# Kernel tuning notes

Hardware: AMD Instinct MI355X
Metric: run time of the kernel (lower is better)

Reference implementation:

```python
import math
import jax, jax.numpy as jnp
import numpy as np

N_HEAD = 16
ROPE_BASE = 10000.0

def setup_inputs() -> dict:
    key = jax.random.key(0)
    k1, k2, k3 = jax.random.split(key, 3)
    B, T, C = 2, 2048, 2048
    x = jax.random.normal(k1, (B, T, C), dtype=jnp.float32)
    Wqkv = jax.random.normal(k2, (C, 3 * C), dtype=jnp.float32) * 0.02  # [C, 3C], y = x @ Wqkv
    Wout = jax.random.normal(k3, (C, C), dtype=jnp.float32) * 0.02
    return {"x": x, "Wqkv": Wqkv, "Wout": Wout}

def _rope_sin_cos(T, half, dtype):
    # build_sin_cos(seq_len, dim=head_size//2): div over arange(0, 2*dim, 2) / (2*dim)
    pos = jnp.arange(T, dtype=jnp.float32)[:, None]                      # [T,1]
    div = jnp.exp(jnp.arange(0, 2 * half, 2, dtype=jnp.float32)
                  * (-math.log(ROPE_BASE) / (2 * half)))                 # [half]
    ang = pos * div                                                      # [T,half]
    return jnp.sin(ang).astype(dtype), jnp.cos(ang).astype(dtype)

def reference(x, Wqkv, Wout):
    B, T, C = x.shape
    H = N_HEAD
    D = C // H
    half = D // 2
    qkv = (x @ Wqkv).reshape(B, T, 3, H, D)
    q, k, v = qkv[:, :, 0], qkv[:, :, 1], qkv[:, :, 2]                   # [B,T,H,D]
    sin, cos = _rope_sin_cos(T, half, x.dtype)
    sin = sin[None, :, None, :]  # [1,T,1,half]
    cos = cos[None, :, None, :]
    def rope(t):
        t1, t2 = t[..., :half], t[..., half:]
        return jnp.concatenate([t1 * cos - t2 * sin, t2 * cos + t1 * sin], axis=-1)
    q, k = rope(q), rope(k)
    scale = 1.0 / math.sqrt(D)  # flash-attn default softmax_scale
    scores = jnp.einsum('bthd,bshd->bhts', q, k) * scale                 # [B,H,T,T]
    causal = jnp.tril(jnp.ones((T, T), dtype=bool))
    scores = jnp.where(causal[None, None], scores, jnp.finfo(scores.dtype).min)
    probs = jax.nn.softmax(scores, axis=-1)
    out = jnp.einsum('bhts,bshd->bhtd', probs, v)                        # [B,H,T,D]
    # Faithful to torch: out.permute(0,2,1,3).reshape(B,T,C) on [B,T,H,D]
    # == flatten of [B,H,T,D] into [B,T,C]
    out = out.reshape(B, T, C)
    return out @ Wout
```

## Files before the change

### kernel.cpp

```cpp
#include <hip/hip_runtime.h>

typedef unsigned short u16;
typedef __attribute__((ext_vector_type(8))) short bf16x8;
typedef __attribute__((ext_vector_type(4))) float f32x4;
typedef __attribute__((ext_vector_type(8))) unsigned short u16x8;

#define B_ 2
#define T_ 2048
#define C_ 2048
#define H_ 16
#define D_ 128
#define QKVW 6144

__device__ __forceinline__ u16 f2b(float f) {
  unsigned int x = __builtin_bit_cast(unsigned int, f);
  x += 0x7fffu + ((x >> 16) & 1u);
  return (u16)(x >> 16);
}
__device__ __forceinline__ float b2f(u16 u) {
  unsigned int x = ((unsigned int)u) << 16;
  return __builtin_bit_cast(float, x);
}
__device__ __forceinline__ void gl_lds16(const void* g, void* l) {
  __builtin_amdgcn_global_load_lds((const __attribute__((address_space(1))) void*)g,
                                   (__attribute__((address_space(3))) void*)l, 16, 0, 0);
}

__global__ void castbf(const float* __restrict__ in, u16* __restrict__ out) {
  int i = blockIdx.x * 256 + threadIdx.x;
  f32x4 a = ((const f32x4*)in)[2 * i];
  f32x4 b = ((const f32x4*)in)[2 * i + 1];
  u16x8 o;
  o[0] = f2b(a[0]); o[1] = f2b(a[1]); o[2] = f2b(a[2]); o[3] = f2b(a[3]);
  o[4] = f2b(b[0]); o[5] = f2b(b[1]); o[6] = f2b(b[2]); o[7] = f2b(b[3]);
  ((u16x8*)out)[i] = o;
}

__global__ __launch_bounds__(256) void castT(const float* __restrict__ in,
                                             u16* __restrict__ out, int K, int N) {
  __shared__ __align__(16) u16 ld[64][72];
  const int nt = blockIdx.x * 64, kt = blockIdx.y * 64;
  const int tid = threadIdx.x;
#pragma unroll
  for (int s = 0; s < 4; ++s) {
    int idx = tid + s * 256;
    int r = idx >> 4;
    int c = (idx & 15) * 4;
    f32x4 v = *(const f32x4*)(in + (size_t)(kt + r) * N + nt + c);
    ld[r][c] = f2b(v[0]); ld[r][c + 1] = f2b(v[1]);
    ld[r][c + 2] = f2b(v[2]); ld[r][c + 3] = f2b(v[3]);
  }
  __syncthreads();
#pragma unroll
  for (int s = 0; s < 2; ++s) {
    int idx = tid + s * 256;
    int n = idx >> 3;
    int c8 = (idx & 7) * 8;
    u16x8 o;
#pragma unroll
    for (int j = 0; j < 8; ++j) o[j] = ld[c8 + j][n];
    *(u16x8*)(out + (size_t)(nt + n) * K + kt + c8) = o;
  }
}

__device__ __forceinline__ void stage_chunk(const u16* __restrict__ g, int K,
                                            u16* l, int ch) {
  int row = ch >> 3;
  int c = (ch & 7) ^ (row & 7);
  gl_lds16(g + (size_t)row * K + c * 8, l + ch * 8);
}

#define MFMA_Q(AF, BF, MH, NH)                                               \
  _Pragma("unroll")                                                          \
  for (int mi = 0; mi < 4; ++mi) {                                           \
    _Pragma("unroll")                                                        \
    for (int ni = 0; ni < 2; ++ni) {                                         \
      _Pragma("unroll")                                                      \
      for (int ks = 0; ks < 2; ++ks)                                         \
        acc[(MH)*4 + mi][(NH)*2 + ni] =                                      \
            __builtin_amdgcn_mfma_f32_16x16x32_bf16(                         \
                AF[mi][ks], BF[ni][ks], acc[(MH)*4 + mi][(NH)*2 + ni],       \
                0, 0, 0);                                                    \
    }                                                                        \
  }

template <int OUT_BF16>
__global__ __launch_bounds__(512, 2) void gemm256(const u16* __restrict__ A,
                                                  const u16* __restrict__ Bt,
                                                  void* __restrict__ Cout,
                                                  int M, int N, int K) {
  __shared__ __align__(16) u16 sm[65536];
  const int tid = threadIdx.x;
  const int lane = tid & 63, w = tid >> 6;
  const int quad = lane >> 4, l15 = lane & 15;
  const int wm = w >> 2, wn = w & 3;
  const int NXT = N >> 8;
  int id = blockIdx.x;
  const int cpx = gridDim.x >> 3;
  id = (id & 7) * cpx + (id >> 3);
  const int tn0 = (id % NXT) * 256, tm0 = (id / NXT) * 256;
  const int NT = K >> 6;
  const u16* Ag = A + (size_t)tm0 * K;
  const u16* Bg = Bt + (size_t)tn0 * K;

  f32x4 acc[8][4] = {};
  bf16x8 a0[4][2], a1[4][2], b0[2][2], b1[2][2];

  auto stA = [&](int tt, int half) {
    u16* l = &sm[(tt & 1) * 32768];
    const u16* g = Ag + tt * 64;
    stage_chunk(g, K, l, half * 512 + tid);
    stage_chunk(g, K, l, 1024 + half * 512 + tid);
  };
  auto stB = [&](int tt, int nh) {
    u16* l = &sm[(tt & 1) * 32768 + 16384];
    const u16* g = Bg + tt * 64;
    int ch = nh * 256 + (tid & 255) + ((tid >> 8) << 9);
    stage_chunk(g, K, l, ch);
    stage_chunk(g, K, l, ch + 1024);
  };

  stA(0, 0); stB(0, 0); stA(0, 1); stB(0, 1);
  if (NT > 1) {
    stA(1, 0); stB(1, 0); stA(1, 1);
    asm volatile("s_waitcnt vmcnt(6)" ::: "memory");
  } else {
    asm volatile("s_waitcnt vmcnt(0)" ::: "memory");
  }
  __builtin_amdgcn_s_barrier();

  for (int t = 0; t < NT; ++t) {
    const u16* LA = &sm[(t & 1) * 32768];
    const u16* LB = LA + 16384;
#pragma unroll
    for (int mi = 0; mi < 4; ++mi)
#pragma unroll
      for (int ks = 0; ks < 2; ++ks) {
        int r = wm * 128 + mi * 16 + l15;
        a0[mi][ks] = *(const bf16x8*)&LA[r * 64 +
                     ((ks * 32 + quad * 8) ^ ((r & 7) << 3))];
      }
#pragma unroll
    for (int ni = 0; ni < 2; ++ni)
#pragma unroll
      for (int ks = 0; ks < 2; ++ks) {
        int r = wn * 64 + ni * 16 + l15;
        b0[ni][ks] = *(const bf16x8*)&LB[r * 64 +
                     ((ks * 32 + quad * 8) ^ ((r & 7) << 3))];
      }
    if (t + 1 < NT) stB(t + 1, 1);
    __builtin_amdgcn_s_barrier();
    asm volatile("s_waitcnt lgkmcnt(0)");
    __builtin_amdgcn_sched_barrier(0);
    __builtin_amdgcn_s_setprio(1);
    MFMA_Q(a0, b0, 0, 0);
    __builtin_amdgcn_s_setprio(0);
    __builtin_amdgcn_s_barrier();
#pragma unroll
    for (int ni = 0; ni < 2; ++ni)
#pragma unroll
      for (int ks = 0; ks < 2; ++ks) {
        int r = wn * 64 + (ni + 2) * 16 + l15;
        b1[ni][ks] = *(const bf16x8*)&LB[r * 64 +
                     ((ks * 32 + quad * 8) ^ ((r & 7) << 3))];
      }
    if (t + 2 < NT) stA(t + 2, 0);
    __builtin_amdgcn_s_barrier();
    asm volatile("s_waitcnt lgkmcnt(0)");
    __builtin_amdgcn_sched_barrier(0);
    __builtin_amdgcn_s_setprio(1);
    MFMA_Q(a0, b1, 0, 1);
    __builtin_amdgcn_s_setprio(0);
    __builtin_amdgcn_s_barrier();
#pragma unroll
    for (int mi = 0; mi < 4; ++mi)
#pragma unroll
      for (int ks = 0; ks < 2; ++ks) {
        int r = wm * 128 + (mi + 4) * 16 + l15;
        a1[mi][ks] = *(const bf16x8*)&LA[r * 64 +
                     ((ks * 32 + quad * 8) ^ ((r & 7) << 3))];
      }
    if (t + 2 < NT) stB(t + 2, 0);
    __builtin_amdgcn_s_barrier();
    asm volatile("s_waitcnt lgkmcnt(0)");
    __builtin_amdgcn_sched_barrier(0);
    __builtin_amdgcn_s_setprio(1);
    MFMA_Q(a1, b1, 1, 1);
    __builtin_amdgcn_s_setprio(0);
    __builtin_amdgcn_s_barrier();
    if (t + 2 < NT) {
      stA(t + 2, 1);
      asm volatile("s_waitcnt vmcnt(6)" ::: "memory");
    } else {
      asm volatile("s_waitcnt vmcnt(0)" ::: "memory");
    }
    __builtin_amdgcn_s_barrier();
    __builtin_amdgcn_s_setprio(1);
    MFMA_Q(a1, b0, 1, 0);
    __builtin_amdgcn_s_setprio(0);
    __builtin_amdgcn_s_barrier();
  }

#pragma unroll
  for (int mi = 0; mi < 8; ++mi)
#pragma unroll
    for (int ni = 0; ni < 4; ++ni)
#pragma unroll
      for (int r = 0; r < 4; ++r) {
        int row = tm0 + wm * 128 + mi * 16 + quad * 4 + r;
        int col = tn0 + wn * 64 + ni * 16 + l15;
        float v = acc[mi][ni][r];
        if (OUT_BF16) ((u16*)Cout)[(size_t)row * N + col] = f2b(v);
        else          ((float*)Cout)[(size_t)row * N + col] = v;
      }
}

__global__ void rope_k(u16* __restrict__ qkv) {
  int g = blockIdx.x * 256 + threadIdx.x;
  int i0 = (g & 7) * 8;
  int h = (g >> 3) & 15;
  int which = (g >> 7) & 1;
  int t = (g >> 8) & 2047;
  int b = g >> 19;
  size_t base = (size_t)(b * T_ + t) * QKVW + which * 2048 + h * 128 + i0;
  u16x8 v1 = *(const u16x8*)(qkv + base);
  u16x8 v2 = *(const u16x8*)(qkv + base + 64);
  u16x8 o1, o2;
#pragma unroll
  for (int j = 0; j < 8; ++j) {
    int i = i0 + j;
    float t1 = b2f(v1[j]), t2 = b2f(v2[j]);
    float ang = (float)t * exp2f(-(float)i * 0.20762050593046439f);
    float sn, cs;
    sincosf(ang, &sn, &cs);
    o1[j] = f2b(t1 * cs - t2 * sn);
    o2[j] = f2b(t2 * cs + t1 * sn);
  }
  *(u16x8*)(qkv + base) = o1;
  *(u16x8*)(qkv + base + 64) = o2;
}

__global__ __launch_bounds__(256) void vtrans(const u16* __restrict__ qkv, u16* __restrict__ vt) {
  __shared__ __align__(16) u16 ld[128][136];
  const int tt = blockIdx.x, bh = blockIdx.y;
  const int b = bh >> 4, h = bh & 15;
  const u16* vb = qkv + (size_t)b * T_ * QKVW + 4096 + h * 128;
  const int tid = threadIdx.x;
#pragma unroll
  for (int s = 0; s < 8; ++s) {
    int t = (tid >> 4) + s * 16;
    int d0 = (tid & 15) * 8;
    *(bf16x8*)&ld[t][d0] = *(const bf16x8*)(vb + (size_t)(tt * 128 + t) * QKVW + d0);
  }
  __syncthreads();
  u16* vout = vt + (size_t)bh * D_ * T_ + tt * 128;
#pragma unroll
  for (int s = 0; s < 8; ++s) {
    int d = (tid >> 4) + s * 16;
    int t0 = (tid & 15) * 8;
    u16x8 o;
#pragma unroll
    for (int j = 0; j < 8; ++j) o[j] = ld[t0 + j][d];
    *(u16x8*)(vout + (size_t)d * T_ + t0) = o;
  }
}

#define APW 72
__global__ __launch_bounds__(256, 2) void attn(const u16* __restrict__ qkv,
                                               const u16* __restrict__ vt,
                                               u16* __restrict__ obuf) {
  __shared__ __align__(16) u16 lK[2][64 * 128];
  __shared__ __align__(16) u16 lV[2][128 * 64];
  __shared__ __align__(16) u16 lP[64 * APW];
  const int tid = threadIdx.x, lane = tid & 63, w = tid >> 6;
  const int quad = lane >> 4, l15 = lane & 15;
  const int bh = blockIdx.x, jp = blockIdx.y;
  const int jA = jp, jB = 31 - jp;
  const int b = bh >> 4, h = bh & 15;
  const u16* qb = qkv + (size_t)b * T_ * QKVW + h * 128;
  const u16* kb = qb + 2048;
  const u16* vtb = vt + (size_t)bh * D_ * T_;

  bf16x8 qfA[4], qfB[4];
#pragma unroll
  for (int kk = 0; kk < 4; ++kk) {
    qfA[kk] = *(const bf16x8*)(qb + (size_t)(jA * 64 + w * 16 + l15) * QKVW + kk * 32 + quad * 8);
    qfB[kk] = *(const bf16x8*)(qb + (size_t)(jB * 64 + w * 16 + l15) * QKVW + kk * 32 + quad * 8);
  }

  f32x4 oA[8] = {}, oB[8] = {};
  float mA[4], lAr[4], mB[4], lBr[4];
#pragma unroll
  for (int r = 0; r < 4; ++r) {
    mA[r] = -__builtin_inff(); lAr[r] = 0.f;
    mB[r] = -__builtin_inff(); lBr[r] = 0.f;
  }
  const float sc = 0.08838834764831845f * 1.4426950408889634f;

  auto stage = [&](int kt, int buf) {
#pragma unroll
    for (int s = 0; s < 4; ++s) {
      int ch = tid + s * 256;
      int kr = ch >> 4, kc = (ch & 15) ^ (kr & 7);
      gl_lds16(kb + (size_t)(kt * 64 + kr) * QKVW + kc * 8, &lK[buf][ch * 8]);
      int vr = ch >> 3, vc = (ch & 7) ^ (vr & 7);
      gl_lds16(vtb + (size_t)vr * T_ + kt * 64 + vc * 8, &lV[buf][ch * 8]);
    }
  };

  auto smpv = [&](f32x4* sacc, f32x4* oacc, float* mrow, float* lrow,
                  int jw, int kt, int cb) {
    const bool diag = (kt == jw);
#pragma unroll
    for (int nj = 0; nj < 4; ++nj) {
      int key = nj * 16 + l15;
#pragma unroll
      for (int r = 0; r < 4; ++r) {
        float s = sacc[nj][r] * sc;
        if (diag) {
          int qrow = w * 16 + quad * 4 + r;
          if (key > qrow) s = -__builtin_inff();
        }
        sacc[nj][r] = s;
      }
    }
    float pm[4];
#pragma unroll
    for (int r = 0; r < 4; ++r)
      pm[r] = fmaxf(fmaxf(sacc[0][r], sacc[1][r]), fmaxf(sacc[2][r], sacc[3][r]));
    float dmax = fmaxf(fmaxf(pm[0] - mrow[0], pm[1] - mrow[1]),
                       fmaxf(pm[2] - mrow[2], pm[3] - mrow[3]));
    if (__any(dmax > 11.5f)) {
#pragma unroll
      for (int r = 0; r < 4; ++r) {
        float rm = pm[r];
        rm = fmaxf(rm, __shfl_xor(rm, 1));
        rm = fmaxf(rm, __shfl_xor(rm, 2));
        rm = fmaxf(rm, __shfl_xor(rm, 4));
        rm = fmaxf(rm, __shfl_xor(rm, 8));
        float mold = mrow[r];
        float mnew = fmaxf(mold, rm);
        float alpha = exp2f(mold - mnew);
#pragma unroll
        for (int nd = 0; nd < 8; ++nd) oacc[nd][r] *= alpha;
        lrow[r] *= alpha;
        mrow[r] = mnew;
      }
    }
#pragma unroll
    for (int r = 0; r < 4; ++r) {
      int prow = w * 16 + quad * 4 + r;
      float rs = 0.f;
#pragma unroll
      for (int nj = 0; nj < 4; ++nj) {
        float p = exp2f(sacc[nj][r] - mrow[r]);
        rs += p;
        lP[prow * APW + nj * 16 + l15] = f2b(p);
      }
      lrow[r] += rs;
    }
#pragma unroll
    for (int kk = 0; kk < 2; ++kk) {
      bf16x8 pf, vf[8];
      pf = *(const bf16x8*)&lP[(w * 16 + l15) * APW + kk * 32 + quad * 8];
#pragma unroll
      for (int nd = 0; nd < 8; ++nd) {
        int r = nd * 16 + l15;
        vf[nd] = *(const bf16x8*)&lV[cb][r * 64 + ((kk * 32 + quad * 8) ^ ((r & 7) << 3))];
      }
      __builtin_amdgcn_s_setprio(1);
#pragma unroll
      for (int nd = 0; nd < 8; ++nd)
        oacc[nd] = __builtin_amdgcn_mfma_f32_16x16x32_bf16(pf, vf[nd], oacc[nd], 0, 0, 0);
      __builtin_amdgcn_s_setprio(0);
    }
  };

  stage(0, 0);
  __syncthreads();

  for (int kt = 0; kt <= jB; ++kt) {
    int cb = kt & 1;
    if (kt < jB) stage(kt + 1, cb ^ 1);
    const bool doA = (kt <= jA);
    f32x4 sB[4] = {}, sA[4] = {};
#pragma unroll
    for (int kk = 0; kk < 4; ++kk) {
      bf16x8 kf[4];
#pragma unroll
      for (int nj = 0; nj < 4; ++nj) {
        int r = nj * 16 + l15;
        kf[nj] = *(const bf16x8*)&lK[cb][r * 128 + ((kk * 32 + quad * 8) ^ ((r & 7) << 3))];
      }
      __builtin_amdgcn_s_setprio(1);
#pragma unroll
      for (int nj = 0; nj < 4; ++nj)
        sB[nj] = __builtin_amdgcn_mfma_f32_16x16x32_bf16(qfB[kk], kf[nj], sB[nj], 0, 0, 0);
      if (doA)
#pragma unroll
        for (int nj = 0; nj < 4; ++nj)
          sA[nj] = __builtin_amdgcn_mfma_f32_16x16x32_bf16(qfA[kk], kf[nj], sA[nj], 0, 0, 0);
      __builtin_amdgcn_s_setprio(0);
    }
    smpv(sB, oB, mB, lBr, jB, kt, cb);
    if (doA) smpv(sA, oA, mA, lAr, jA, kt, cb);
    __syncthreads();
  }

#pragma unroll
  for (int r = 0; r < 4; ++r) {
    float sA = lAr[r], sB = lBr[r];
    sA += __shfl_xor(sA, 1); sB += __shfl_xor(sB, 1);
    sA += __shfl_xor(sA, 2); sB += __shfl_xor(sB, 2);
    sA += __shfl_xor(sA, 4); sB += __shfl_xor(sB, 4);
    sA += __shfl_xor(sA, 8); sB += __shfl_xor(sB, 8);
    lAr[r] = sA; lBr[r] = sB;
  }

#pragma unroll
  for (int nd = 0; nd < 8; ++nd)
#pragma unroll
    for (int r = 0; r < 4; ++r) {
      int dcol = nd * 16 + l15;
      int qrB = jB * 64 + w * 16 + quad * 4 + r;
      obuf[((size_t)bh * T_ + qrB) * D_ + dcol] = f2b(oB[nd][r] / lBr[r]);
      int qrA = jA * 64 + w * 16 + quad * 4 + r;
      obuf[((size_t)bh * T_ + qrA) * D_ + dcol] = f2b(oA[nd][r] / lAr[r]);
    }
}

extern "C" void kernel_launch(void* const* d_in, const int* in_sizes, int n_in,
                              void* d_out, int out_size, void* d_ws, size_t ws_size,
                              hipStream_t stream) {
  const float* x = (const float*)d_in[0];
  const float* Wqkv = (const float*)d_in[1];
  const float* Wout = (const float*)d_in[2];
  float* out = (float*)d_out;
  char* ws = (char*)d_ws;

  u16* xb   = (u16*)ws;
  u16* wqt  = (u16*)(ws + 16777216);
  u16* qkvb = (u16*)(ws + 41943040);
  u16* vtb  = (u16*)(ws + 92274688);
  u16* wot  = wqt;
  u16* ob   = xb;

  castbf<<<4096, 256, 0, stream>>>(x, xb);
  castT<<<dim3(96, 32), 256, 0, stream>>>(Wqkv, wqt, 2048, 6144);
  gemm256<1><<<dim3(384), 512, 0, stream>>>(xb, wqt, qkvb, 4096, 6144, 2048);
  castT<<<dim3(32, 32), 256, 0, stream>>>(Wout, wot, 2048, 2048);
  rope_k<<<4096, 256, 0, stream>>>(qkvb);
  vtrans<<<dim3(16, 32), 256, 0, stream>>>(qkvb, vtb);
  attn<<<dim3(32, 16), 256, 0, stream>>>(qkvb, vtb, ob);
  gemm256<0><<<dim3(128), 512, 0, stream>>>(ob, wot, out, 4096, 2048, 2048);
}
```

Baseline: 400.7 us.

## Add 128x256-tile GEMM variant to balance wave quantization across CUs

Adds a new gemmH kernel using 128x256 output tiles with a triple-buffered LDS pipeline. The QKV projection is split into a 256x256-tile launch covering the first 4096 columns and a gemmH launch covering the remaining 2048 columns. The output projection moves from 128 large-tile blocks to 256 half-height blocks. The goal is to fill all CUs with whole waves of blocks instead of leaving some idle in a partial last wave. In exchange, the smaller tiles reuse each loaded operand less, and splitting the QKV GEMM adds a kernel launch.

Measured after the change: 376.0 us. 1.07x faster.

```diff
diff --git a/kernel.cpp b/kernel.cpp
--- a/kernel.cpp
+++ b/kernel.cpp
@@ -88,17 +88,16 @@
 __global__ __launch_bounds__(512, 2) void gemm256(const u16* __restrict__ A,
                                                   const u16* __restrict__ Bt,
                                                   void* __restrict__ Cout,
-                                                  int M, int N, int K) {
+                                                  int M, int N, int K, int NTILE) {
   __shared__ __align__(16) u16 sm[65536];
   const int tid = threadIdx.x;
   const int lane = tid & 63, w = tid >> 6;
   const int quad = lane >> 4, l15 = lane & 15;
   const int wm = w >> 2, wn = w & 3;
-  const int NXT = N >> 8;
   int id = blockIdx.x;
   const int cpx = gridDim.x >> 3;
   id = (id & 7) * cpx + (id >> 3);
-  const int tn0 = (id % NXT) * 256, tm0 = (id / NXT) * 256;
+  const int tn0 = (id % NTILE) * 256, tm0 = (id / NTILE) * 256;
   const int NT = K >> 6;
   const u16* Ag = A + (size_t)tm0 * K;
   const u16* Bg = Bt + (size_t)tn0 * K;
@@ -210,6 +209,128 @@
         int row = tm0 + wm * 128 + mi * 16 + quad * 4 + r;
         int col = tn0 + wn * 64 + ni * 16 + l15;
         float v = acc[mi][ni][r];
+        if (OUT_BF16) ((u16*)Cout)[(size_t)row * N + col] = f2b(v);
+        else          ((float*)Cout)[(size_t)row * N + col] = v;
+      }
+}
+
+template <int OUT_BF16>
+__global__ __launch_bounds__(512, 2) void gemmH(const u16* __restrict__ A,
+                                                const u16* __restrict__ Bt,
+                                                void* __restrict__ Cout,
+                                                int M, int N, int K,
+                                                int NTILE, int tnbase) {
+  __shared__ __align__(16) u16 sm[3][24576];
+  const int tid = threadIdx.x;
+  const int lane = tid & 63, w = tid >> 6;
+  const int quad = lane >> 4, l15 = lane & 15;
+  const int wm = w >> 2, wn = w & 3;
+  int id = blockIdx.x;
+  const int cpx = gridDim.x >> 3;
+  id = (id & 7) * cpx + (id >> 3);
+  const int tn0 = tnbase + (id % NTILE) * 256, tm0 = (id / NTILE) * 128;
+  const int NT = K >> 6;
+  const u16* Ag = A + (size_t)tm0 * K;
+  const u16* Bg = Bt + (size_t)tn0 * K;
+
+  f32x4 acc[4][4] = {};
+  bf16x8 af[4][2], b0[2][2], b1[2][2];
+
+  auto stage6 = [&](int tt) {
+    u16* l = sm[tt % 3];
+    const u16* g = Ag + tt * 64;
+    stage_chunk(g, K, l, tid);
+    stage_chunk(g, K, l, 512 + tid);
+    const u16* gb = Bg + tt * 64;
+#pragma unroll
+    for (int h = 0; h < 2; ++h)
+#pragma unroll
+      for (int s = 0; s < 2; ++s) {
+        int ch = s * 512 + tid;
+        int ru = ch >> 3, cc = ch & 7;
+        int row = ((ru >> 5) << 6) + h * 32 + (ru & 31);
+        int csrc = cc ^ (ru & 7);
+        gl_lds16(gb + (size_t)row * K + csrc * 8, &l[8192 + h * 8192 + ch * 8]);
+      }
+  };
+
+  stage6(0);
+  if (NT > 1) {
+    stage6(1);
+    asm volatile("s_waitcnt vmcnt(6)" ::: "memory");
+  } else {
+    asm volatile("s_waitcnt vmcnt(0)" ::: "memory");
+  }
+  __builtin_amdgcn_s_barrier();
+
+  for (int t = 0; t < NT; ++t) {
+    const u16* L = sm[t % 3];
+#pragma unroll
+    for (int mi = 0; mi < 4; ++mi)
+#pragma unroll
+      for (int ks = 0; ks < 2; ++ks) {
+        int r = wm * 64 + mi * 16 + l15;
+        af[mi][ks] = *(const bf16x8*)&L[r * 64 +
+                     ((ks * 32 + quad * 8) ^ ((r & 7) << 3))];
+      }
+#pragma unroll
+    for (int nj = 0; nj < 2; ++nj)
+#pragma unroll
+      for (int ks = 0; ks < 2; ++ks) {
+        int ru = wn * 32 + nj * 16 + l15;
+        b0[nj][ks] = *(const bf16x8*)&L[8192 + ru * 64 +
+                     ((ks * 32 + quad * 8) ^ ((ru & 7) << 3))];
+      }
+    if (t + 2 < NT) stage6(t + 2);
+    __builtin_amdgcn_s_barrier();
+    asm volatile("s_waitcnt lgkmcnt(0)");
+    __builtin_amdgcn_sched_barrier(0);
+    __builtin_amdgcn_s_setprio(1);
+#pragma unroll
+    for (int mi = 0; mi < 4; ++mi)
+#pragma unroll
+      for (int nj = 0; nj < 2; ++nj)
+#pragma unroll
+        for (int ks = 0; ks < 2; ++ks)
+          acc[mi][nj] = __builtin_amdgcn_mfma_f32_16x16x32_bf16(af[mi][ks], b0[nj][ks], acc[mi][nj], 0, 0, 0);
+    __builtin_amdgcn_s_setprio(0);
+    __builtin_amdgcn_s_barrier();
+#pragma unroll
+    for (int nj = 0; nj < 2; ++nj)
+#pragma unroll
+      for (int ks = 0; ks < 2; ++ks) {
+        int ru = wn * 32 + nj * 16 + l15;
+        b1[nj][ks] = *(const bf16x8*)&L[16384 + ru * 64 +
+                     ((ks * 32 + quad * 8) ^ ((ru & 7) << 3))];
+      }
+    if (t + 2 < NT)
+      asm volatile("s_waitcnt vmcnt(6)" ::: "memory");
+    else
+      asm volatile("s_waitcnt vmcnt(0)" ::: "memory");
+    __builtin_amdgcn_s_barrier();
+    asm volatile("s_waitcnt lgkmcnt(0)");
+    __builtin_amdgcn_sched_barrier(0);
+    __builtin_amdgcn_s_setprio(1);
+#pragma unroll
+    for (int mi = 0; mi < 4; ++mi)
+#pragma unroll
+      for (int nj = 0; nj < 2; ++nj)
+#pragma unroll
+        for (int ks = 0; ks < 2; ++ks)
+          acc[mi][nj + 2] = __builtin_amdgcn_mfma_f32_16x16x32_bf16(af[mi][ks], b1[nj][ks], acc[mi][nj + 2], 0, 0, 0);
+    __builtin_amdgcn_s_setprio(0);
+    __builtin_amdgcn_s_barrier();
+  }
+
+#pragma unroll
+  for (int mi = 0; mi < 4; ++mi)
+#pragma unroll
+    for (int nj = 0; nj < 4; ++nj)
+#pragma unroll
+      for (int r = 0; r < 4; ++r) {
+        int row = tm0 + wm * 64 + mi * 16 + quad * 4 + r;
+        int col = tn0 + wn * 64 + nj * 16 + l15;
+        float v = acc[mi][nj][r];
         if (OUT_BF16) ((u16*)Cout)[(size_t)row * N + col] = f2b(v);
         else          ((float*)Cout)[(size_t)row * N + col] = v;
       }
@@ -447,10 +568,11 @@
 
   castbf<<<4096, 256, 0, stream>>>(x, xb);
   castT<<<dim3(96, 32), 256, 0, stream>>>(Wqkv, wqt, 2048, 6144);
-  gemm256<1><<<dim3(384), 512, 0, stream>>>(xb, wqt, qkvb, 4096, 6144, 2048);
+  gemm256<1><<<dim3(256), 512, 0, stream>>>(xb, wqt, qkvb, 4096, 6144, 2048, 16);
+  gemmH<1><<<dim3(256), 512, 0, stream>>>(xb, wqt, qkvb, 4096, 6144, 2048, 8, 4096);
   castT<<<dim3(32, 32), 256, 0, stream>>>(Wout, wot, 2048, 2048);
   rope_k<<<4096, 256, 0, stream>>>(qkvb);
   vtrans<<<dim3(16, 32), 256, 0, stream>>>(qkvb, vtb);
   attn<<<dim3(32, 16), 256, 0, stream>>>(qkvb, vtb, ob);
-  gemm256<0><<<dim3(128), 512, 0, stream>>>(ob, wot, out, 4096, 2048, 2048);
-}
+  gemmH<0><<<dim3(256), 512, 0, stream>>>(ob, wot, out, 4096, 2048, 2048, 8, 0);
+}
```
